# Kernel tuning notes

Measured on AMD Instinct MI355X. Metric: run time of the kernel, lower is better.

## Reference

```python
import jax, jax.numpy as jnp
import numpy as np

B, N, D, H = 8192, 9, 1024, 4096
# query_type '3p': num_layer=3, edges (h_ind, r_ind, t_ind), no negation, simple_graph=False
EDGES = [(2, 3, 4), (4, 5, 6), (6, 7, 8)]
NUM_LAYER = 3
EPS = 0.1


def setup_inputs() -> dict:
    key = jax.random.key(0)
    k1, k2, k3 = jax.random.split(key, 3)
    scale1 = 1.0 / np.sqrt(D)
    scale2 = 1.0 / np.sqrt(H)
    return {
        "node_embedding": jax.random.normal(k1, (B, N, D), dtype=jnp.float32),
        "W1": jax.random.normal(k2, (D, H), dtype=jnp.float32) * scale1,
        "b1": jnp.zeros((H,), dtype=jnp.float32),
        "W2": jax.random.normal(k3, (H, D), dtype=jnp.float32) * scale2,
        "b2": jnp.zeros((D,), dtype=jnp.float32),
    }


def reference(node_embedding, W1, b1, W2, b2):
    # message passing: for each edge, tail gets estimate_tail(h, r) = h + r,
    # head gets estimate_head(t, r) = t - r (mp_lhs=True, mp_rel=False).
    # The num_layer loop re-appends identical messages, so sum = NUM_LAYER * per-edge sum.
    msgs = {}
    for h, r, t in EDGES:
        he = node_embedding[:, h]   # [B, D]
        re_ = node_embedding[:, r]
        te = node_embedding[:, t]
        msgs.setdefault(t, []).append(he + re_)   # estimate_tail_emb
        msgs.setdefault(h, []).append(te - re_)   # estimate_head_emb

    def mlp(x):
        return jax.nn.relu(x @ W1 + b1) @ W2 + b2

    terms = sorted(msgs.keys())  # [2, 4, 6, 8] for '3p'
    outs = []
    for t in terms:
        agg = NUM_LAYER * sum(msgs[t]) + node_embedding[:, t] * EPS  # agg_func='sum'
        outs.append(mlp(agg))
    return jnp.stack(outs, axis=0)  # [num_terms, B, D]
```

## Files before the change

kernel.cpp:

```cpp
#include <hip/hip_runtime.h>
#include <hip/hip_bf16.h>

typedef __hip_bfloat16 bf16;
typedef __attribute__((ext_vector_type(8))) short short8;
typedef __attribute__((ext_vector_type(4))) short short4v;
typedef __attribute__((ext_vector_type(16))) float floatx16;

#define BQ 8192
#define ND 9
#define DD 1024
#define HH 4096
#define MM 32768

__device__ __forceinline__ short f2bf(float f) {
  unsigned u = __float_as_uint(f);
  u = (u + 0x7fff + ((u >> 16) & 1)) >> 16;
  return (short)u;
}

__device__ __forceinline__ void async16(const void* g, void* l) {
  __builtin_amdgcn_global_load_lds(
      (const __attribute__((address_space(1))) void*)g,
      (__attribute__((address_space(3))) void*)l, 16, 0, 0);
}

__global__ __launch_bounds__(256) void build_x(const float* __restrict__ emb,
                                               bf16* __restrict__ X) {
  int b = blockIdx.x;
  int d = threadIdx.x * 4;
  const float* base = emb + (size_t)b * (ND * DD) + d;

  float e[7][4];
#pragma unroll
  for (int k = 0; k < 7; ++k) *(float4*)e[k] = *(const float4*)(base + (k + 2) * DD);

  auto store = [&](int t, const float* v) {
    short4v o;
#pragma unroll
    for (int c = 0; c < 4; ++c) o[c] = f2bf(v[c]);
    *(short4v*)(X + ((size_t)t * BQ + b) * DD + d) = o;
  };

  float o0[4], o1[4], o2[4], o3[4];
#pragma unroll
  for (int c = 0; c < 4; ++c) {
    o0[c] = 0.1f * e[0][c] - 3.f * e[1][c] + 3.f * e[2][c];
    o1[c] = 3.f * e[0][c] + 3.f * e[1][c] + 0.1f * e[2][c] - 3.f * e[3][c] + 3.f * e[4][c];
    o2[c] = 3.f * e[2][c] + 3.f * e[3][c] + 0.1f * e[4][c] - 3.f * e[5][c] + 3.f * e[6][c];
    o3[c] = 3.f * e[4][c] + 3.f * e[5][c] + 0.1f * e[6][c];
  }
  store(0, o0); store(1, o1); store(2, o2); store(3, o3);
}

__global__ void transpose_f2b(const float* __restrict__ src, bf16* __restrict__ dst,
                              int rows, int cols) {
  __shared__ float t[32][33];
  int c0 = blockIdx.x * 32, r0 = blockIdx.y * 32;
  int tx = threadIdx.x, ty = threadIdx.y;
  t[ty][tx] = src[(size_t)(r0 + ty) * cols + (c0 + tx)];
  __syncthreads();
  short v = f2bf(t[tx][ty]);
  dst[(size_t)(c0 + ty) * rows + (r0 + tx)] = *(bf16*)&v;
}

template <int RELU, typename OutT>
__global__ __launch_bounds__(256) void gemm_bt(const bf16* __restrict__ A,
                                               const bf16* __restrict__ Bt,
                                               const float* __restrict__ bias,
                                               OutT* __restrict__ C,
                                               int M, int N, int K, int lognx) {
  __shared__ bf16 As[128 * 64];
  __shared__ bf16 Bs[128 * 64];
  int tid = threadIdx.x;
  int lane = tid & 63;
  int wave = tid >> 6;
  int wm = wave >> 1, wn = wave & 1;

  int G = gridDim.x * gridDim.y;
  int b = blockIdx.y * gridDim.x + blockIdx.x;
  int gb = (b & 7) * (G >> 3) + (b >> 3);
  int ntile = gb & ((1 << lognx) - 1);
  int mtile = gb >> lognx;
  int m0 = mtile * 128, n0 = ntile * 128;

  floatx16 acc[2][2];
#pragma unroll
  for (int i = 0; i < 2; ++i)
#pragma unroll
    for (int j = 0; j < 2; ++j)
#pragma unroll
      for (int r = 0; r < 16; ++r) acc[i][j][r] = 0.f;

  int srow = lane >> 3;
  int scol = ((lane & 7) ^ srow) * 8;

  const bf16* ga[4];
  const bf16* gb_[4];
#pragma unroll
  for (int j = 0; j < 4; ++j) {
    int row = (wave * 4 + j) * 8 + srow;
    ga[j] = A + (size_t)(m0 + row) * K + scol;
    gb_[j] = Bt + (size_t)(n0 + row) * K + scol;
  }

  int rr = lane & 7;
  int mrow = wm * 64 + (lane & 31);
  int nrow = wn * 64 + (lane & 31);
  int half = lane >> 5;

  for (int k0 = 0; k0 < K; k0 += 64) {
#pragma unroll
    for (int j = 0; j < 4; ++j) {
      int q = wave * 4 + j;
      async16(ga[j], (char*)As + q * 1024);
      async16(gb_[j], (char*)Bs + q * 1024);
      ga[j] += 64;
      gb_[j] += 64;
    }
    __syncthreads();

#pragma unroll
    for (int ks = 0; ks < 64; ks += 16) {
      int sl = (ks >> 3) + half;
      int ps = (sl ^ rr) << 3;
      short8 af[2], bf[2];
#pragma unroll
      for (int i = 0; i < 2; ++i)
        af[i] = *(const short8*)(As + (mrow + i * 32) * 64 + ps);
#pragma unroll
      for (int j = 0; j < 2; ++j)
        bf[j] = *(const short8*)(Bs + (nrow + j * 32) * 64 + ps);
#pragma unroll
      for (int i = 0; i < 2; ++i)
#pragma unroll
        for (int j = 0; j < 2; ++j)
          acc[i][j] = __builtin_amdgcn_mfma_f32_32x32x16_bf16(af[i], bf[j], acc[i][j], 0, 0, 0);
    }
    __syncthreads();
  }

  int colbase = n0 + wn * 64 + (lane & 31);
  int rowbase = m0 + wm * 64 + 4 * half;
#pragma unroll
  for (int j = 0; j < 2; ++j) {
    int col = colbase + j * 32;
    float bv = bias[col];
#pragma unroll
    for (int i = 0; i < 2; ++i) {
#pragma unroll
      for (int r = 0; r < 16; ++r) {
        int row = rowbase + i * 32 + (r & 3) + 8 * (r >> 2);
        float v = acc[i][j][r] + bv;
        if (RELU) v = fmaxf(v, 0.f);
        if constexpr (sizeof(OutT) == 2) {
          short s = f2bf(v);
          C[(size_t)row * N + col] = *(OutT*)&s;
        } else {
          C[(size_t)row * N + col] = *(OutT*)&v;
        }
      }
    }
  }
}

extern "C" void kernel_launch(void* const* d_in, const int* in_sizes, int n_in,
                              void* d_out, int out_size, void* d_ws, size_t ws_size,
                              hipStream_t stream) {
  const float* emb = (const float*)d_in[0];
  const float* W1  = (const float*)d_in[1];
  const float* b1  = (const float*)d_in[2];
  const float* W2  = (const float*)d_in[3];
  const float* b2  = (const float*)d_in[4];
  float* out = (float*)d_out;

  char* ws = (char*)d_ws;
  bf16* X   = (bf16*)(ws);
  bf16* Y   = (bf16*)(ws + (size_t)67108864);
  bf16* W1t = (bf16*)(ws + (size_t)67108864 + (size_t)268435456);
  bf16* W2t = (bf16*)(ws + (size_t)67108864 + (size_t)268435456 + (size_t)8388608);

  build_x<<<dim3(BQ), dim3(256), 0, stream>>>(emb, X);
  transpose_f2b<<<dim3(HH / 32, DD / 32), dim3(32, 32), 0, stream>>>(W1, W1t, DD, HH);
  transpose_f2b<<<dim3(DD / 32, HH / 32), dim3(32, 32), 0, stream>>>(W2, W2t, HH, DD);
  gemm_bt<1, bf16><<<dim3(HH / 128, MM / 128), dim3(256), 0, stream>>>(X, W1t, b1, Y, MM, HH, DD, 5);
  gemm_bt<0, float><<<dim3(DD / 128, MM / 128), dim3(256), 0, stream>>>(Y, W2t, b2, out, MM, DD, HH, 3);
}
```

Before: 1.161 ms.

## Replace 128x128 GEMM with 256x256 double-buffered, quadrant-pipelined MFMA kernel

Replaces the simple 128x128-tile GEMM, which loaded a tile and then synchronised before every step, with a 256x256-tile kernel using 512 threads, a 128KB double-buffered LDS ring and 16x16x32 MFMAs. The K loop is split into four quadrant phases, and async global-to-LDS loads for upcoming tiles are interleaved with the MFMA work using explicit vmcnt/lgkmcnt waits and s_setprio. The aim is to hide global load latency and raise per-block data reuse. In exchange it uses far more LDS and registers per block, which lowers occupancy, and the hand-written waitcnt scheduling is fragile.

```diff
diff --git a/kernel.cpp b/kernel.cpp
--- a/kernel.cpp
+++ b/kernel.cpp
@@ -4,7 +4,7 @@
 typedef __hip_bfloat16 bf16;
 typedef __attribute__((ext_vector_type(8))) short short8;
 typedef __attribute__((ext_vector_type(4))) short short4v;
-typedef __attribute__((ext_vector_type(16))) float floatx16;
+typedef __attribute__((ext_vector_type(4))) float floatx4;
 
 #define BQ 8192
 #define ND 9
@@ -63,104 +63,158 @@
   dst[(size_t)(c0 + ty) * rows + (r0 + tx)] = *(bf16*)&v;
 }
 
-template <int RELU, typename OutT>
-__global__ __launch_bounds__(256) void gemm_bt(const bf16* __restrict__ A,
-                                               const bf16* __restrict__ Bt,
-                                               const float* __restrict__ bias,
-                                               OutT* __restrict__ C,
-                                               int M, int N, int K, int lognx) {
-  __shared__ bf16 As[128 * 64];
-  __shared__ bf16 Bs[128 * 64];
-  int tid = threadIdx.x;
-  int lane = tid & 63;
-  int wave = tid >> 6;
-  int wm = wave >> 1, wn = wave & 1;
-
-  int G = gridDim.x * gridDim.y;
-  int b = blockIdx.y * gridDim.x + blockIdx.x;
-  int gb = (b & 7) * (G >> 3) + (b >> 3);
-  int ntile = gb & ((1 << lognx) - 1);
-  int mtile = gb >> lognx;
-  int m0 = mtile * 128, n0 = ntile * 128;
-
-  floatx16 acc[2][2];
-#pragma unroll
-  for (int i = 0; i < 2; ++i)
-#pragma unroll
-    for (int j = 0; j < 2; ++j)
-#pragma unroll
-      for (int r = 0; r < 16; ++r) acc[i][j][r] = 0.f;
-
-  int srow = lane >> 3;
-  int scol = ((lane & 7) ^ srow) * 8;
-
-  const bf16* ga[4];
-  const bf16* gb_[4];
-#pragma unroll
-  for (int j = 0; j < 4; ++j) {
-    int row = (wave * 4 + j) * 8 + srow;
-    ga[j] = A + (size_t)(m0 + row) * K + scol;
-    gb_[j] = Bt + (size_t)(n0 + row) * K + scol;
+template <int RELU, typename OutT, int K, int N, int LOGNX>
+__global__ __launch_bounds__(512, 2) void gemm256(const bf16* __restrict__ A,
+                                                  const bf16* __restrict__ Bt,
+                                                  const float* __restrict__ bias,
+                                                  OutT* __restrict__ C) {
+  constexpr int NT = K / 64;
+  __shared__ bf16 sm[65536];
+  char* smc = (char*)sm;
+  const bf16* smb = (const bf16*)sm;
+
+  const int tid = threadIdx.x;
+  const int l = tid & 63;
+  const int wv = tid >> 6;
+
+  const int G = gridDim.x;
+  const int b = blockIdx.x;
+  const int gb = (b & 7) * (G >> 3) + (b >> 3);
+  const int n0 = (gb & ((1 << LOGNX) - 1)) * 256;
+  const int m0 = (gb >> LOGNX) * 256;
+
+  const int rowb = wv * 8 + (l >> 3);
+  const int kx = ((l & 7) ^ ((l >> 3) & 7)) << 3;
+  const bf16* pA = A + (size_t)(m0 + rowb) * K + kx;
+  const bf16* pB = Bt + (size_t)(n0 + rowb) * K + kx;
+  const int wlo = wv * 1024;
+
+  const int ra = ((wv >> 1) * 32 + (l & 15)) * 64;
+  const int rb = ((wv & 1) * 64 + (l & 15)) * 64;
+  const int kg = l >> 4;
+  const int sx = l & 7;
+
+  floatx4 acc[4][8];
+#pragma unroll
+  for (int q = 0; q < 4; ++q)
+#pragma unroll
+    for (int f = 0; f < 8; ++f)
+#pragma unroll
+      for (int r = 0; r < 4; ++r) acc[q][f][r] = 0.f;
+
+#define STG(GP, LO)                                            \
+  do {                                                         \
+    async16((GP), smc + (LO) + wlo);                           \
+    async16((GP) + (size_t)64 * K, smc + (LO) + wlo + 8192);   \
+  } while (0)
+
+#define LOAD_A(HOFF)                                                          \
+  _Pragma("unroll") for (int mf = 0; mf < 2; ++mf)                            \
+  _Pragma("unroll") for (int ks = 0; ks < 2; ++ks)                            \
+      a[mf][ks] = *(const short8*)(smb + bufe + (HOFF) + ra + mf * 1024 +     \
+                                   ((((ks << 2) + kg) ^ sx) << 3));
+
+#define LOAD_B(HOFF)                                                          \
+  _Pragma("unroll") for (int nf = 0; nf < 4; ++nf)                            \
+  _Pragma("unroll") for (int ks = 0; ks < 2; ++ks)                            \
+      bfr[nf][ks] = *(const short8*)(smb + bufe + (HOFF) + rb + nf * 1024 +   \
+                                     ((((ks << 2) + kg) ^ sx) << 3));
+
+#define MFMA16(Q)                                                             \
+  __builtin_amdgcn_s_setprio(1);                                              \
+  _Pragma("unroll") for (int ks = 0; ks < 2; ++ks)                            \
+  _Pragma("unroll") for (int mf = 0; mf < 2; ++mf)                            \
+  _Pragma("unroll") for (int nf = 0; nf < 4; ++nf)                            \
+      acc[Q][mf * 4 + nf] = __builtin_amdgcn_mfma_f32_16x16x32_bf16(          \
+          a[mf][ks], bfr[nf][ks], acc[Q][mf * 4 + nf], 0, 0, 0);              \
+  __builtin_amdgcn_s_setprio(0);
+
+#define BAR() __builtin_amdgcn_s_barrier()
+#define LGKM0() asm volatile("s_waitcnt lgkmcnt(0)" ::: "memory")
+#define VM4() asm volatile("s_waitcnt vmcnt(4)" ::: "memory")
+#define VM0() asm volatile("s_waitcnt vmcnt(0)" ::: "memory")
+
+  STG(pB, 32768);
+  STG(pA + (size_t)128 * K, 16384);
+  STG(pA, 0);
+  STG(pB + (size_t)128 * K, 49152);
+  STG(pB + 64, 65536 + 32768);
+  STG(pA + (size_t)128 * K + 64, 65536 + 16384);
+  VM4();
+  BAR();
+
+  for (int t = 0; t < NT; ++t) {
+    const int bufe = (t & 1) << 15;
+    const int bufn = ((t + 1) & 1) << 16;
+    const int bufc = (t & 1) << 16;
+    short8 a[2][2], bfr[4][2];
+
+    LOAD_A(0);
+    LOAD_B(16384);
+    if (t + 1 < NT) STG(pA + (size_t)(t + 1) * 64, bufn);
+    BAR();
+    LGKM0();
+    MFMA16(0);
+    BAR();
+
+    LOAD_A(8192);
+    if (t + 1 < NT) STG(pB + (size_t)128 * K + (size_t)(t + 1) * 64, bufn + 49152);
+    BAR();
+    LGKM0();
+    MFMA16(1);
+    BAR();
+
+    LOAD_B(24576);
+    if (t + 2 < NT) STG(pB + (size_t)(t + 2) * 64, bufc + 32768);
+    BAR();
+    LGKM0();
+    MFMA16(2);
+    BAR();
+
+    LOAD_A(0);
+    if (t + 2 < NT) STG(pA + (size_t)128 * K + (size_t)(t + 2) * 64, bufc + 16384);
+    BAR();
+    LGKM0();
+    MFMA16(3);
+    if (t + 2 < NT) { VM4(); } else { VM0(); }
+    BAR();
   }
 
-  int rr = lane & 7;
-  int mrow = wm * 64 + (lane & 31);
-  int nrow = wn * 64 + (lane & 31);
-  int half = lane >> 5;
-
-  for (int k0 = 0; k0 < K; k0 += 64) {
-#pragma unroll
-    for (int j = 0; j < 4; ++j) {
-      int q = wave * 4 + j;
-      async16(ga[j], (char*)As + q * 1024);
-      async16(gb_[j], (char*)Bs + q * 1024);
-      ga[j] += 64;
-      gb_[j] += 64;
-    }
-    __syncthreads();
-
-#pragma unroll
-    for (int ks = 0; ks < 64; ks += 16) {
-      int sl = (ks >> 3) + half;
-      int ps = (sl ^ rr) << 3;
-      short8 af[2], bf[2];
-#pragma unroll
-      for (int i = 0; i < 2; ++i)
-        af[i] = *(const short8*)(As + (mrow + i * 32) * 64 + ps);
-#pragma unroll
-      for (int j = 0; j < 2; ++j)
-        bf[j] = *(const short8*)(Bs + (nrow + j * 32) * 64 + ps);
-#pragma unroll
-      for (int i = 0; i < 2; ++i)
-#pragma unroll
-        for (int j = 0; j < 2; ++j)
-          acc[i][j] = __builtin_amdgcn_mfma_f32_32x32x16_bf16(af[i], bf[j], acc[i][j], 0, 0, 0);
-    }
-    __syncthreads();
-  }
-
-  int colbase = n0 + wn * 64 + (lane & 31);
-  int rowbase = m0 + wm * 64 + 4 * half;
-#pragma unroll
-  for (int j = 0; j < 2; ++j) {
-    int col = colbase + j * 32;
-    float bv = bias[col];
-#pragma unroll
-    for (int i = 0; i < 2; ++i) {
-#pragma unroll
-      for (int r = 0; r < 16; ++r) {
-        int row = rowbase + i * 32 + (r & 3) + 8 * (r >> 2);
-        float v = acc[i][j][r] + bv;
-        if (RELU) v = fmaxf(v, 0.f);
-        if constexpr (sizeof(OutT) == 2) {
-          short s = f2bf(v);
-          C[(size_t)row * N + col] = *(OutT*)&s;
-        } else {
-          C[(size_t)row * N + col] = *(OutT*)&v;
+  const int col0 = n0 + (wv & 1) * 64 + (l & 15);
+  const int row0 = m0 + (wv >> 1) * 32 + ((l >> 4) << 2);
+#pragma unroll
+  for (int q = 0; q < 4; ++q) {
+    const int qa = (q == 1 || q == 2) ? 1 : 0;
+    const int qb = (q >= 2) ? 1 : 0;
+#pragma unroll
+    for (int nf = 0; nf < 4; ++nf) {
+      const int col = col0 + qb * 128 + nf * 16;
+      const float bv = bias[col];
+#pragma unroll
+      for (int mf = 0; mf < 2; ++mf) {
+#pragma unroll
+        for (int r = 0; r < 4; ++r) {
+          const int row = row0 + qa * 128 + mf * 16 + r;
+          float v = acc[q][mf * 4 + nf][r] + bv;
+          if (RELU) v = fmaxf(v, 0.f);
+          if constexpr (sizeof(OutT) == 2) {
+            short s = f2bf(v);
+            C[(size_t)row * N + col] = *(OutT*)&s;
+          } else {
+            C[(size_t)row * N + col] = *(OutT*)&v;
+          }
         }
       }
     }
   }
+#undef STG
+#undef LOAD_A
+#undef LOAD_B
+#undef MFMA16
+#undef BAR
+#undef LGKM0
+#undef VM4
+#undef VM0
 }
 
 extern "C" void kernel_launch(void* const* d_in, const int* in_sizes, int n_in,
@@ -182,6 +236,6 @@
   build_x<<<dim3(BQ), dim3(256), 0, stream>>>(emb, X);
   transpose_f2b<<<dim3(HH / 32, DD / 32), dim3(32, 32), 0, stream>>>(W1, W1t, DD, HH);
   transpose_f2b<<<dim3(DD / 32, HH / 32), dim3(32, 32), 0, stream>>>(W2, W2t, HH, DD);
-  gemm_bt<1, bf16><<<dim3(HH / 128, MM / 128), dim3(256), 0, stream>>>(X, W1t, b1, Y, MM, HH, DD, 5);
-  gemm_bt<0, float><<<dim3(DD / 128, MM / 128), dim3(256), 0, stream>>>(Y, W2t, b2, out, MM, DD, HH, 3);
-}
+  gemm256<1, bf16, DD, HH, 4><<<dim3((MM / 256) * (HH / 256)), dim3(512), 0, stream>>>(X, W1t, b1, Y);
+  gemm256<0, float, HH, DD, 2><<<dim3((MM / 256) * (DD / 256)), dim3(512), 0, stream>>>(Y, W2t, b2, out);
+}
```

After: 930.2 us. 1.25x faster.
